# Kernel optimization log

Hardware: AMD Instinct MI355X
Metric: run time of the kernel (lower is better)

The kernel has to match this reference:

```python
import jax, jax.numpy as jnp
import numpy as np

M = 9           # n_views
CENTER = M // 2 # int(M/2)


def _grid_sample_zeros(img, gx, gy):
    """PyTorch F.grid_sample(mode='bilinear', padding_mode='zeros', align_corners=False).
    img: [V,B,H,W,C]; gx,gy: [V,B,H,W,N] normalized coords in [-1,1] (x=width, y=height).
    Returns [V,B,H,W,N,C]."""
    V, B, H, W, C = img.shape
    ix = ((gx + 1.0) * W - 1.0) * 0.5   # unnormalize, align_corners=False
    iy = ((gy + 1.0) * H - 1.0) * 0.5
    x0 = jnp.floor(ix).astype(jnp.int32); x1 = x0 + 1
    y0 = jnp.floor(iy).astype(jnp.int32); y1 = y0 + 1
    wx1 = ix - x0; wx0 = 1.0 - wx1
    wy1 = iy - y0; wy0 = 1.0 - wy1
    v_idx = jnp.arange(V)[:, None, None, None, None]
    b_idx = jnp.arange(B)[None, :, None, None, None]

    def corner(xi, yi, w):
        valid = (xi >= 0) & (xi < W) & (yi >= 0) & (yi < H)
        xc = jnp.clip(xi, 0, W - 1)
        yc = jnp.clip(yi, 0, H - 1)
        vals = img[v_idx, b_idx, yc, xc]            # [V,B,H,W,N,C] irregular gather
        return vals * (w * valid.astype(img.dtype))[..., None]

    return (corner(x0, y0, wx0 * wy0) + corner(x1, y0, wx1 * wy0)
            + corner(x0, y1, wx0 * wy1) + corner(x1, y1, wx1 * wy1))


def _forward(deltmap, imageMxM, x_g, conv_w, conv_b):
    B, H, W, N = deltmap.shape
    C = imageMxM.shape[3]
    V = M * M
    # base grid: linspace(-1,1) (matches torch code which passes it to align_corners=False sampling)
    base_x = jnp.linspace(-1.0, 1.0, W)[None, :] * jnp.ones((H, 1))   # [H,W]
    base_y = jnp.linspace(-1.0, 1.0, H)[:, None] * jnp.ones((1, W))   # [H,W]
    # per-view offsets; flatten views v-major (v outer loop, u inner) as in the torch code
    uu = jnp.tile(jnp.arange(M), M)      # [V] u varies fastest
    vv = jnp.repeat(jnp.arange(M), M)    # [V]
    sx = (2.0 * (CENTER - uu) / W).astype(deltmap.dtype)  # [V]
    sy = (2.0 * (CENTER - vv) / H).astype(deltmap.dtype)
    gx = base_x[None, None, :, :, None] + sx[:, None, None, None, None] * deltmap[None]  # [V,B,H,W,N]
    gy = base_y[None, None, :, :, None] + sy[:, None, None, None, None] * deltmap[None]
    # images per view: [B,H,W,C,M,M] -> [M,M,B,H,W,C] -> [V,B,H,W,C]
    img = jnp.moveaxis(imageMxM, (4, 5), (0, 1)).reshape(V, B, H, W, C)
    sampled = _grid_sample_zeros(img, gx, gy)          # [V,B,H,W,N,C]
    # cost layout [B,C,V,H,W,N], gate with x_g [B,1,H,W,V] -> [B,1,V,H,W,1]
    cost = jnp.transpose(sampled, (1, 5, 0, 2, 3, 4))  # [B,C,V,H,W,N]
    gate = jnp.transpose(x_g, (0, 1, 4, 2, 3))[..., None]
    cost = (cost * gate).reshape(B, C * V, H, W, N)    # channel order: c-major then v (matches reshape)
    out = jnp.einsum('bkhwn,ok->bohwn', cost, conv_w) + conv_b[None, :, None, None, None]
    return out  # [B, output_dim, H, W, N]


def setup_inputs() -> dict:
    key = jax.random.key(0)
    k1, k2, k3, k4, k5 = jax.random.split(key, 5)
    B, H, W, N, C, OUT = 1, 128, 128, 4, 8, 64
    V = M * M
    deltmap = jax.random.normal(k1, (B, H, W, N), dtype=jnp.float32)
    imageMxM = jax.random.normal(k2, (B, H, W, C, M, M), dtype=jnp.float32)
    x_g = jax.random.uniform(k3, (B, 1, H, W, V), dtype=jnp.float32)
    fan_in = C * V
    bound = 1.0 / np.sqrt(fan_in)
    conv_w = jax.random.uniform(k4, (OUT, fan_in), minval=-bound, maxval=bound, dtype=jnp.float32)
    conv_b = jax.random.uniform(k5, (OUT,), minval=-bound, maxval=bound, dtype=jnp.float32)
    return {"deltmap": deltmap, "imageMxM": imageMxM, "x_g": x_g, "conv_w": conv_w, "conv_b": conv_b}


def reference(deltmap, imageMxM, x_g, conv_w, conv_b):
    return _forward(deltmap, imageMxM, x_g, conv_w, conv_b)
```

## Files before the change

kernel.cpp:

```cpp
#include <hip/hip_runtime.h>

typedef __attribute__((ext_vector_type(8))) short bhalf8_t;
typedef __attribute__((ext_vector_type(4))) float f32x4_t;

#define KCHUNKS 21
#define NPOS 65536
#define NBLK 1024
#define W_BYTES 172032
#define T_BYTES 42467328
#define VIEW_FLOATS 131072
#define CHUNK_BYTES (4 * VIEW_FLOATS * 4)

__global__ __launch_bounds__(256) void prep_w_kernel(
    const float* __restrict__ cw, unsigned short* __restrict__ WtP)
{
    __shared__ float row[648];
    const int o = blockIdx.x, t = threadIdx.x;
    for (int i = t; i < 648; i += 256) row[i] = cw[o * 648 + i];
    __syncthreads();
    for (int k = t; k < 672; k += 256) {
        const int v = k >> 3, c = k & 7;
        const float val = (v < 81) ? row[c * 81 + v] : 0.0f;
        const unsigned int hb = __float_as_uint(val) & 0xffff0000u;
        const float r = val - __uint_as_float(hb);
        const unsigned int lb = __float_as_uint(r) & 0xffff0000u;
        const int kc = k >> 5, g = (k >> 3) & 3, e = k & 7;
        const int ix = kc * 4096 + g * 512 + o * 8 + e;
        WtP[ix]        = (unsigned short)(hb >> 16);
        WtP[ix + 2048] = (unsigned short)(lb >> 16);
    }
}

__global__ __launch_bounds__(256) void prep_T_all(
    const float* __restrict__ img, float* __restrict__ T)
{
    __shared__ float tile[16 * 8 * 85];
    const int b = blockIdx.x, t = threadIdx.x;
    const int y = b >> 3, xs = (b & 7) << 4;
    const float* src = img + (size_t)(y * 128 + xs) * 648;
#pragma unroll
    for (int k = 0; k < 64; ++k) {
        const int i = t + k * 256;
        const int vi = i & 127;
        const int c = (i >> 7) & 7;
        const int x = i >> 10;
        if (vi < 81)
            tile[(x * 8 + c) * 85 + vi] = src[x * 648 + c * 81 + vi];
    }
    __syncthreads();
#pragma unroll
    for (int k = 0; k < 64; ++k) {
        const int i = t + k * 256;
        const int vi = i >> 7;
        const int x = (i >> 3) & 15;
        const int c = i & 7;
        if (vi < 81)
            T[((size_t)(vi * 128 + y) * 128 + xs + x) * 8 + c] =
                tile[(x * 8 + c) * 85 + vi];
    }
}

__global__ __launch_bounds__(256) void prep_T_pass(
    const float* __restrict__ img, float* __restrict__ T, int v0, int nv)
{
    __shared__ float tile[16 * 8 * 85];
    const int b = blockIdx.x, t = threadIdx.x;
    const int y = b >> 3, xs = (b & 7) << 4;
    const int total = 16 * 8 * nv;
    const float* src = img + (size_t)(y * 128 + xs) * 648;
    for (int i = t; i < total; i += 256) {
        const int x = i / (8 * nv);
        const int rem = i - x * (8 * nv);
        const int c = rem / nv;
        const int vi = rem - c * nv;
        tile[(x * 8 + c) * 85 + vi] = src[x * 648 + c * 81 + v0 + vi];
    }
    __syncthreads();
    for (int i = t; i < total; i += 256) {
        const int vi = i >> 7;
        const int x = (i >> 3) & 15;
        const int c = i & 7;
        T[((size_t)(vi * 128 + y) * 128 + xs + x) * 8 + c] = tile[(x * 8 + c) * 85 + vi];
    }
}

__device__ inline unsigned int pack_pair(float a, float b, unsigned int& lw)
{
    const unsigned int ha = __float_as_uint(a) & 0xffff0000u;
    const unsigned int hb = __float_as_uint(b) & 0xffff0000u;
    const float ra = a - __uint_as_float(ha);
    const float rb = b - __uint_as_float(hb);
    lw = (__float_as_uint(ra) >> 16) | (__float_as_uint(rb) & 0xffff0000u);
    return (ha >> 16) | hb;
}

__device__ inline bhalf8_t to_b8(unsigned int a, unsigned int b,
                                 unsigned int c, unsigned int d)
{
    union { uint4 q; bhalf8_t h; } u;
    u.q = make_uint4(a, b, c, d);
    return u.h;
}

__global__ __launch_bounds__(256, 4) void build_reg(
    const float* __restrict__ delt, const float* __restrict__ xg,
    const float* __restrict__ T, const unsigned short* __restrict__ WtP,
    const float* __restrict__ bias, float* __restrict__ out,
    int kc0, int nkc, int first)
{
    const int t = threadIdx.x;
    const int frow = t & 15;
    const int fg = (t >> 4) & 3;
    const int wv = t >> 6;
    const int pos = blockIdx.x * 64 + wv * 16 + frow;
    const int h = pos >> 9;
    const int w = (pos >> 2) & 127;

    const float dlt = delt[pos];
    const float ix0 = fmaf((float)w, 128.0f / 127.0f, -0.5f);
    const float iy0 = fmaf((float)h, 128.0f / 127.0f, -0.5f);
    const int xgbase = (h * 128 + w) * 81;

    f32x4_t acc[4];
#pragma unroll
    for (int j = 0; j < 4; ++j) acc[j] = (f32x4_t)0.0f;

    for (int ci = 0; ci < nkc; ++ci) {
        const int kc = kc0 + ci;
        const int v = kc * 4 + fg;
        float sc0=0.f,sc1=0.f,sc2=0.f,sc3=0.f,sc4=0.f,sc5=0.f,sc6=0.f,sc7=0.f;
        float gate = 0.0f;
        if (v < 81) {
            gate = xg[xgbase + v];
            const int uu = v % 9, vv = v / 9;
            const float ix = fmaf((float)(4 - uu), dlt, ix0);
            const float iy = fmaf((float)(4 - vv), dlt, iy0);
            const float x0f = floorf(ix), y0f = floorf(iy);
            const float wx1 = ix - x0f, wy1 = iy - y0f;
            const float wx0 = 1.0f - wx1, wy0 = 1.0f - wy1;
            const int x0 = (int)x0f, y0 = (int)y0f;
            const int x1 = x0 + 1, y1 = y0 + 1;
            const float ex0 = (x0 >= 0 && x0 < 128) ? wx0 : 0.0f;
            const float ex1 = (x1 >= 0 && x1 < 128) ? wx1 : 0.0f;
            const float ey0 = (y0 >= 0 && y0 < 128) ? wy0 : 0.0f;
            const float ey1 = (y1 >= 0 && y1 < 128) ? wy1 : 0.0f;
            const int xc0 = min(max(x0, 0), 127), xc1 = min(max(x1, 0), 127);
            const int yc0 = min(max(y0, 0), 127), yc1 = min(max(y1, 0), 127);
            const float* bv = T + (size_t)(ci * 4 + fg) * VIEW_FLOATS;
            const float4* p00 = (const float4*)(bv + (yc0 * 128 + xc0) * 8);
            const float4* p01 = (const float4*)(bv + (yc0 * 128 + xc1) * 8);
            const float4* p10 = (const float4*)(bv + (yc1 * 128 + xc0) * 8);
            const float4* p11 = (const float4*)(bv + (yc1 * 128 + xc1) * 8);
            const float w00 = ex0 * ey0, w01 = ex1 * ey0;
            const float w10 = ex0 * ey1, w11 = ex1 * ey1;
            const float4 a00 = p00[0], b00 = p00[1];
            const float4 a01 = p01[0], b01 = p01[1];
            const float4 a10 = p10[0], b10 = p10[1];
            const float4 a11 = p11[0], b11 = p11[1];
            sc0 = fmaf(w11, a11.x, fmaf(w10, a10.x, fmaf(w01, a01.x, w00 * a00.x)));
            sc1 = fmaf(w11, a11.y, fmaf(w10, a10.y, fmaf(w01, a01.y, w00 * a00.y)));
            sc2 = fmaf(w11, a11.z, fmaf(w10, a10.z, fmaf(w01, a01.z, w00 * a00.z)));
            sc3 = fmaf(w11, a11.w, fmaf(w10, a10.w, fmaf(w01, a01.w, w00 * a00.w)));
            sc4 = fmaf(w11, b11.x, fmaf(w10, b10.x, fmaf(w01, b01.x, w00 * b00.x)));
            sc5 = fmaf(w11, b11.y, fmaf(w10, b10.y, fmaf(w01, b01.y, w00 * b00.y)));
            sc6 = fmaf(w11, b11.z, fmaf(w10, b10.z, fmaf(w01, b01.z, w00 * b00.z)));
            sc7 = fmaf(w11, b11.w, fmaf(w10, b10.w, fmaf(w01, b01.w, w00 * b00.w)));
        }
        const float g0 = sc0 * gate, g1 = sc1 * gate, g2 = sc2 * gate, g3 = sc3 * gate;
        const float g4 = sc4 * gate, g5 = sc5 * gate, g6 = sc6 * gate, g7 = sc7 * gate;
        unsigned int lw0, lw1, lw2, lw3;
        const unsigned int hw0 = pack_pair(g0, g1, lw0);
        const unsigned int hw1 = pack_pair(g2, g3, lw1);
        const unsigned int hw2 = pack_pair(g4, g5, lw2);
        const unsigned int hw3 = pack_pair(g6, g7, lw3);
        const bhalf8_t fa_hi = to_b8(hw0, hw1, hw2, hw3);
        const bhalf8_t fa_lo = to_b8(lw0, lw1, lw2, lw3);

        const unsigned short* wbase = WtP + kc * 4096 + fg * 512;
        bhalf8_t fw_hi[4], fw_lo[4];
#pragma unroll
        for (int j = 0; j < 4; ++j) {
            const int o = j * 16 + frow;
            fw_hi[j] = *(const bhalf8_t*)(wbase + o * 8);
            fw_lo[j] = *(const bhalf8_t*)(wbase + 2048 + o * 8);
        }
#pragma unroll
        for (int j = 0; j < 4; ++j) {
            acc[j] = __builtin_amdgcn_mfma_f32_16x16x32_bf16(fa_hi, fw_hi[j], acc[j], 0, 0, 0);
            acc[j] = __builtin_amdgcn_mfma_f32_16x16x32_bf16(fa_lo, fw_hi[j], acc[j], 0, 0, 0);
            acc[j] = __builtin_amdgcn_mfma_f32_16x16x32_bf16(fa_hi, fw_lo[j], acc[j], 0, 0, 0);
        }
    }

    const int posb = blockIdx.x * 64 + wv * 16 + fg * 4;
#pragma unroll
    for (int j = 0; j < 4; ++j) {
        const int o = j * 16 + frow;
        float* dst = out + (size_t)o * NPOS + posb;
        if (first) {
            const float bb = bias[o];
            *(float4*)dst = make_float4(acc[j][0] + bb, acc[j][1] + bb,
                                        acc[j][2] + bb, acc[j][3] + bb);
        } else {
            float4 cur = *(const float4*)dst;
            *(float4*)dst = make_float4(cur.x + acc[j][0], cur.y + acc[j][1],
                                        cur.z + acc[j][2], cur.w + acc[j][3]);
        }
    }
}

__global__ __launch_bounds__(256) void build_direct(
    const float* __restrict__ delt, const float* __restrict__ xg,
    const float* __restrict__ img, const float* __restrict__ cw,
    const float* __restrict__ bias, float* __restrict__ out)
{
    const int t = threadIdx.x;
    const int frow = t & 15;
    const int fg = (t >> 4) & 3;
    const int wv = t >> 6;
    const int pos = blockIdx.x * 64 + wv * 16 + frow;
    const int h = pos >> 9;
    const int w = (pos >> 2) & 127;

    const float dlt = delt[pos];
    const float ix0 = fmaf((float)w, 128.0f / 127.0f, -0.5f);
    const float iy0 = fmaf((float)h, 128.0f / 127.0f, -0.5f);
    const int xgbase = (h * 128 + w) * 81;

    f32x4_t acc[4];
#pragma unroll
    for (int j = 0; j < 4; ++j) acc[j] = (f32x4_t)0.0f;

    for (int kc = 0; kc < KCHUNKS; ++kc) {
        const int v = kc * 4 + fg;
        float sc[8];
#pragma unroll
        for (int c = 0; c < 8; ++c) sc[c] = 0.0f;
        float gate = 0.0f;
        if (v < 81) {
            gate = xg[xgbase + v];
            const int uu = v % 9, vv = v / 9;
            const float ix = fmaf((float)(4 - uu), dlt, ix0);
            const float iy = fmaf((float)(4 - vv), dlt, iy0);
            const float x0f = floorf(ix), y0f = floorf(iy);
            const float wx1 = ix - x0f, wy1 = iy - y0f;
            const float wx0 = 1.0f - wx1, wy0 = 1.0f - wy1;
            const int x0 = (int)x0f, y0 = (int)y0f;
            const int x1 = x0 + 1, y1 = y0 + 1;
            const float ex0 = (x0 >= 0 && x0 < 128) ? wx0 : 0.0f;
            const float ex1 = (x1 >= 0 && x1 < 128) ? wx1 : 0.0f;
            const float ey0 = (y0 >= 0 && y0 < 128) ? wy0 : 0.0f;
            const float ey1 = (y1 >= 0 && y1 < 128) ? wy1 : 0.0f;
            const int xc0 = min(max(x0, 0), 127), xc1 = min(max(x1, 0), 127);
            const int yc0 = min(max(y0, 0), 127), yc1 = min(max(y1, 0), 127);
            const float cwt[4] = {ex0 * ey0, ex1 * ey0, ex0 * ey1, ex1 * ey1};
            const int cyx[4] = {yc0 * 128 + xc0, yc0 * 128 + xc1,
                                yc1 * 128 + xc0, yc1 * 128 + xc1};
#pragma unroll
            for (int k = 0; k < 4; ++k) {
                const float* p = img + (size_t)cyx[k] * 648 + v;
#pragma unroll
                for (int c = 0; c < 8; ++c)
                    sc[c] = fmaf(cwt[k], p[c * 81], sc[c]);
            }
        }
        unsigned int hw[4], lw[4];
#pragma unroll
        for (int q = 0; q < 4; ++q)
            hw[q] = pack_pair(sc[2 * q] * gate, sc[2 * q + 1] * gate, lw[q]);
        const bhalf8_t fa_hi = to_b8(hw[0], hw[1], hw[2], hw[3]);
        const bhalf8_t fa_lo = to_b8(lw[0], lw[1], lw[2], lw[3]);

        bhalf8_t fw_hi[4], fw_lo[4];
#pragma unroll
        for (int j = 0; j < 4; ++j) {
            const int o = j * 16 + frow;
#pragma unroll
            for (int e = 0; e < 8; ++e) {
                const float val = (v < 81) ? cw[o * 648 + e * 81 + v] : 0.0f;
                const unsigned int hb = __float_as_uint(val) & 0xffff0000u;
                const float r = val - __uint_as_float(hb);
                fw_hi[j][e] = (short)(hb >> 16);
                fw_lo[j][e] = (short)(__float_as_uint(r) >> 16);
            }
        }
#pragma unroll
        for (int j = 0; j < 4; ++j) {
            acc[j] = __builtin_amdgcn_mfma_f32_16x16x32_bf16(fa_hi, fw_hi[j], acc[j], 0, 0, 0);
            acc[j] = __builtin_amdgcn_mfma_f32_16x16x32_bf16(fa_lo, fw_hi[j], acc[j], 0, 0, 0);
            acc[j] = __builtin_amdgcn_mfma_f32_16x16x32_bf16(fa_hi, fw_lo[j], acc[j], 0, 0, 0);
        }
    }

    const int posb = blockIdx.x * 64 + wv * 16 + fg * 4;
#pragma unroll
    for (int j = 0; j < 4; ++j) {
        const int o = j * 16 + frow;
        const float bb = bias[o];
        float* dst = out + (size_t)o * NPOS + posb;
        *(float4*)dst = make_float4(acc[j][0] + bb, acc[j][1] + bb,
                                    acc[j][2] + bb, acc[j][3] + bb);
    }
}

extern "C" void kernel_launch(void* const* d_in, const int* in_sizes, int n_in,
                              void* d_out, int out_size, void* d_ws, size_t ws_size,
                              hipStream_t stream)
{
    const float* deltmap = (const float*)d_in[0];
    const float* image   = (const float*)d_in[1];
    const float* xgp     = (const float*)d_in[2];
    const float* cw      = (const float*)d_in[3];
    const float* cb      = (const float*)d_in[4];
    float* outp = (float*)d_out;

    unsigned short* WtP = (unsigned short*)d_ws;
    float* T = (float*)((char*)d_ws + W_BYTES);

    const bool okT = ws_size >= (size_t)W_BYTES + T_BYTES;

    if (okT) {
        prep_w_kernel<<<64, 256, 0, stream>>>(cw, WtP);
        prep_T_all<<<1024, 256, 0, stream>>>(image, T);
        build_reg<<<NBLK, 256, 0, stream>>>(deltmap, xgp, T, WtP, cb, outp,
                                            0, KCHUNKS, 1);
    } else {
        long long availT = (long long)ws_size - (long long)W_BYTES;
        int G = 0;
        if (availT > 0) {
            long long g = availT / CHUNK_BYTES;
            G = (g > 21) ? 21 : (int)g;
        }
        if (G >= 1) {
            prep_w_kernel<<<64, 256, 0, stream>>>(cw, WtP);
            int first = 1;
            for (int kc0 = 0; kc0 < KCHUNKS; kc0 += G) {
                const int nkc = (KCHUNKS - kc0 < G) ? (KCHUNKS - kc0) : G;
                const int v0 = kc0 * 4;
                int nv = 81 - v0;
                if (nv > nkc * 4) nv = nkc * 4;
                prep_T_pass<<<1024, 256, 0, stream>>>(image, T, v0, nv);
                build_reg<<<NBLK, 256, 0, stream>>>(deltmap, xgp, T, WtP, cb, outp,
                                                    kc0, nkc, first);
                first = 0;
            }
        } else {
            build_direct<<<NBLK, 256, 0, stream>>>(deltmap, xgp, image, cw, cb, outp);
        }
    }
}
```

Before: 184.1 us.

## Add software-pipelined build kernel that prefetches next chunk's gathers during MFMA

Adds a build_pipe kernel where each 128-thread block handles 32 positions. Every thread gathers one view for one position, then writes the packed bf16 hi/lo fragments into double-buffered shared memory. The next chunk's bilinear gathers are issued before the current chunk's MFMAs so that memory latency overlaps matrix math, and the per-thread work is no longer split by view group. This costs a __syncthreads and shared-memory traffic per chunk, plus more registers to hold the in-flight gather results.

Measured after the change: 189.1 us. +2.7%, slower.

```diff
diff --git a/kernel.cpp b/kernel.cpp
--- a/kernel.cpp
+++ b/kernel.cpp
@@ -5,7 +5,6 @@
 
 #define KCHUNKS 21
 #define NPOS 65536
-#define NBLK 1024
 #define W_BYTES 172032
 #define T_BYTES 42467328
 #define VIEW_FLOATS 131072
@@ -102,6 +101,141 @@
     return u.h;
 }
 
+struct GatherRegs {
+    float4 a00, b00, a01, b01, a10, b10, a11, b11;
+    float w00, w01, w10, w11, gate;
+};
+
+__device__ inline void gather_issue(int v, float dlt, float ix0, float iy0,
+    int xgbase, const float* __restrict__ xg, const float* __restrict__ T,
+    GatherRegs& g)
+{
+    const int vc = (v < 81) ? v : 80;
+    g.gate = (v < 81) ? xg[xgbase + v] : 0.0f;
+    const int uu = vc % 9, vv = vc / 9;
+    const float ix = fmaf((float)(4 - uu), dlt, ix0);
+    const float iy = fmaf((float)(4 - vv), dlt, iy0);
+    const float x0f = floorf(ix), y0f = floorf(iy);
+    const float wx1 = ix - x0f, wy1 = iy - y0f;
+    const float wx0 = 1.0f - wx1, wy0 = 1.0f - wy1;
+    const int x0 = (int)x0f, y0 = (int)y0f;
+    const int x1 = x0 + 1, y1 = y0 + 1;
+    const float ex0 = (x0 >= 0 && x0 < 128) ? wx0 : 0.0f;
+    const float ex1 = (x1 >= 0 && x1 < 128) ? wx1 : 0.0f;
+    const float ey0 = (y0 >= 0 && y0 < 128) ? wy0 : 0.0f;
+    const float ey1 = (y1 >= 0 && y1 < 128) ? wy1 : 0.0f;
+    const int xc0 = min(max(x0, 0), 127), xc1 = min(max(x1, 0), 127);
+    const int yc0 = min(max(y0, 0), 127), yc1 = min(max(y1, 0), 127);
+    g.w00 = ex0 * ey0; g.w01 = ex1 * ey0;
+    g.w10 = ex0 * ey1; g.w11 = ex1 * ey1;
+    const float* bv = T + (size_t)vc * VIEW_FLOATS;
+    const float4* p00 = (const float4*)(bv + (yc0 * 128 + xc0) * 8);
+    const float4* p01 = (const float4*)(bv + (yc0 * 128 + xc1) * 8);
+    const float4* p10 = (const float4*)(bv + (yc1 * 128 + xc0) * 8);
+    const float4* p11 = (const float4*)(bv + (yc1 * 128 + xc1) * 8);
+    g.a00 = p00[0]; g.b00 = p00[1];
+    g.a01 = p01[0]; g.b01 = p01[1];
+    g.a10 = p10[0]; g.b10 = p10[1];
+    g.a11 = p11[0]; g.b11 = p11[1];
+}
+
+__device__ inline void gather_consume(const GatherRegs& g, uint4& hi, uint4& lo)
+{
+    const float s0 = fmaf(g.w11, g.a11.x, fmaf(g.w10, g.a10.x, fmaf(g.w01, g.a01.x, g.w00 * g.a00.x)));
+    const float s1 = fmaf(g.w11, g.a11.y, fmaf(g.w10, g.a10.y, fmaf(g.w01, g.a01.y, g.w00 * g.a00.y)));
+    const float s2 = fmaf(g.w11, g.a11.z, fmaf(g.w10, g.a10.z, fmaf(g.w01, g.a01.z, g.w00 * g.a00.z)));
+    const float s3 = fmaf(g.w11, g.a11.w, fmaf(g.w10, g.a10.w, fmaf(g.w01, g.a01.w, g.w00 * g.a00.w)));
+    const float s4 = fmaf(g.w11, g.b11.x, fmaf(g.w10, g.b10.x, fmaf(g.w01, g.b01.x, g.w00 * g.b00.x)));
+    const float s5 = fmaf(g.w11, g.b11.y, fmaf(g.w10, g.b10.y, fmaf(g.w01, g.b01.y, g.w00 * g.b00.y)));
+    const float s6 = fmaf(g.w11, g.b11.z, fmaf(g.w10, g.b10.z, fmaf(g.w01, g.b01.z, g.w00 * g.b00.z)));
+    const float s7 = fmaf(g.w11, g.b11.w, fmaf(g.w10, g.b10.w, fmaf(g.w01, g.b01.w, g.w00 * g.b00.w)));
+    unsigned int lw0, lw1, lw2, lw3;
+    const unsigned int hw0 = pack_pair(s0 * g.gate, s1 * g.gate, lw0);
+    const unsigned int hw1 = pack_pair(s2 * g.gate, s3 * g.gate, lw1);
+    const unsigned int hw2 = pack_pair(s4 * g.gate, s5 * g.gate, lw2);
+    const unsigned int hw3 = pack_pair(s6 * g.gate, s7 * g.gate, lw3);
+    hi = make_uint4(hw0, hw1, hw2, hw3);
+    lo = make_uint4(lw0, lw1, lw2, lw3);
+}
+
+__global__ __launch_bounds__(128, 4) void build_pipe(
+    const float* __restrict__ delt, const float* __restrict__ xg,
+    const float* __restrict__ T, const unsigned short* __restrict__ WtP,
+    const float* __restrict__ bias, float* __restrict__ out)
+{
+    __shared__ __align__(16) unsigned short Ahi[2][4][32][8];
+    __shared__ __align__(16) unsigned short Alo[2][4][32][8];
+
+    const int t = threadIdx.x;
+    const int wv = t >> 6;
+    const int lane = t & 63;
+    const int sg = t >> 5;
+    const int sp = t & 31;
+    const int pos_s = blockIdx.x * 32 + sp;
+    const int h_s = pos_s >> 9;
+    const int w_s = (pos_s >> 2) & 127;
+    const float dlt = delt[pos_s];
+    const float ix0 = fmaf((float)w_s, 128.0f / 127.0f, -0.5f);
+    const float iy0 = fmaf((float)h_s, 128.0f / 127.0f, -0.5f);
+    const int xgbase = (h_s * 128 + w_s) * 81;
+
+    const int frow = lane & 15;
+    const int fg = lane >> 4;
+
+    f32x4_t acc[4];
+#pragma unroll
+    for (int j = 0; j < 4; ++j) acc[j] = (f32x4_t)0.0f;
+
+    uint4 hiN, loN;
+    {
+        GatherRegs gr;
+        gather_issue(sg, dlt, ix0, iy0, xgbase, xg, T, gr);
+        gather_consume(gr, hiN, loN);
+    }
+
+    for (int ci = 0; ci < KCHUNKS; ++ci) {
+        const int cur = ci & 1;
+        *(uint4*)(&Ahi[cur][sg][sp][0]) = hiN;
+        *(uint4*)(&Alo[cur][sg][sp][0]) = loN;
+        __syncthreads();
+
+        GatherRegs gr;
+        const bool have = (ci + 1 < KCHUNKS);
+        if (have)
+            gather_issue((ci + 1) * 4 + sg, dlt, ix0, iy0, xgbase, xg, T, gr);
+
+        const int r = wv * 16 + frow;
+        const bhalf8_t fa_hi = *(const bhalf8_t*)(&Ahi[cur][fg][r][0]);
+        const bhalf8_t fa_lo = *(const bhalf8_t*)(&Alo[cur][fg][r][0]);
+        const unsigned short* wbase = WtP + ci * 4096 + fg * 512;
+        bhalf8_t fw_hi[4], fw_lo[4];
+#pragma unroll
+        for (int j = 0; j < 4; ++j) {
+            const int o = j * 16 + frow;
+            fw_hi[j] = *(const bhalf8_t*)(wbase + o * 8);
+            fw_lo[j] = *(const bhalf8_t*)(wbase + 2048 + o * 8);
+        }
+#pragma unroll
+        for (int j = 0; j < 4; ++j) {
+            acc[j] = __builtin_amdgcn_mfma_f32_16x16x32_bf16(fa_hi, fw_hi[j], acc[j], 0, 0, 0);
+            acc[j] = __builtin_amdgcn_mfma_f32_16x16x32_bf16(fa_lo, fw_hi[j], acc[j], 0, 0, 0);
+            acc[j] = __builtin_amdgcn_mfma_f32_16x16x32_bf16(fa_hi, fw_lo[j], acc[j], 0, 0, 0);
+        }
+
+        if (have) gather_consume(gr, hiN, loN);
+    }
+
+    const int posb = blockIdx.x * 32 + wv * 16 + fg * 4;
+#pragma unroll
+    for (int j = 0; j < 4; ++j) {
+        const int o = j * 16 + frow;
+        const float bb = bias[o];
+        float* dst = out + (size_t)o * NPOS + posb;
+        *(float4*)dst = make_float4(acc[j][0] + bb, acc[j][1] + bb,
+                                    acc[j][2] + bb, acc[j][3] + bb);
+    }
+}
+
 __global__ __launch_bounds__(256, 4) void build_reg(
     const float* __restrict__ delt, const float* __restrict__ xg,
     const float* __restrict__ T, const unsigned short* __restrict__ WtP,
@@ -128,53 +262,13 @@
     for (int ci = 0; ci < nkc; ++ci) {
         const int kc = kc0 + ci;
         const int v = kc * 4 + fg;
-        float sc0=0.f,sc1=0.f,sc2=0.f,sc3=0.f,sc4=0.f,sc5=0.f,sc6=0.f,sc7=0.f;
-        float gate = 0.0f;
-        if (v < 81) {
-            gate = xg[xgbase + v];
-            const int uu = v % 9, vv = v / 9;
-            const float ix = fmaf((float)(4 - uu), dlt, ix0);
-            const float iy = fmaf((float)(4 - vv), dlt, iy0);
-            const float x0f = floorf(ix), y0f = floorf(iy);
-            const float wx1 = ix - x0f, wy1 = iy - y0f;
-            const float wx0 = 1.0f - wx1, wy0 = 1.0f - wy1;
-            const int x0 = (int)x0f, y0 = (int)y0f;
-            const int x1 = x0 + 1, y1 = y0 + 1;
-            const float ex0 = (x0 >= 0 && x0 < 128) ? wx0 : 0.0f;
-            const float ex1 = (x1 >= 0 && x1 < 128) ? wx1 : 0.0f;
-            const float ey0 = (y0 >= 0 && y0 < 128) ? wy0 : 0.0f;
-            const float ey1 = (y1 >= 0 && y1 < 128) ? wy1 : 0.0f;
-            const int xc0 = min(max(x0, 0), 127), xc1 = min(max(x1, 0), 127);
-            const int yc0 = min(max(y0, 0), 127), yc1 = min(max(y1, 0), 127);
-            const float* bv = T + (size_t)(ci * 4 + fg) * VIEW_FLOATS;
-            const float4* p00 = (const float4*)(bv + (yc0 * 128 + xc0) * 8);
-            const float4* p01 = (const float4*)(bv + (yc0 * 128 + xc1) * 8);
-            const float4* p10 = (const float4*)(bv + (yc1 * 128 + xc0) * 8);
-            const float4* p11 = (const float4*)(bv + (yc1 * 128 + xc1) * 8);
-            const float w00 = ex0 * ey0, w01 = ex1 * ey0;
-            const float w10 = ex0 * ey1, w11 = ex1 * ey1;
-            const float4 a00 = p00[0], b00 = p00[1];
-            const float4 a01 = p01[0], b01 = p01[1];
-            const float4 a10 = p10[0], b10 = p10[1];
-            const float4 a11 = p11[0], b11 = p11[1];
-            sc0 = fmaf(w11, a11.x, fmaf(w10, a10.x, fmaf(w01, a01.x, w00 * a00.x)));
-            sc1 = fmaf(w11, a11.y, fmaf(w10, a10.y, fmaf(w01, a01.y, w00 * a00.y)));
-            sc2 = fmaf(w11, a11.z, fmaf(w10, a10.z, fmaf(w01, a01.z, w00 * a00.z)));
-            sc3 = fmaf(w11, a11.w, fmaf(w10, a10.w, fmaf(w01, a01.w, w00 * a00.w)));
-            sc4 = fmaf(w11, b11.x, fmaf(w10, b10.x, fmaf(w01, b01.x, w00 * b00.x)));
-            sc5 = fmaf(w11, b11.y, fmaf(w10, b10.y, fmaf(w01, b01.y, w00 * b00.y)));
-            sc6 = fmaf(w11, b11.z, fmaf(w10, b10.z, fmaf(w01, b01.z, w00 * b00.z)));
-            sc7 = fmaf(w11, b11.w, fmaf(w10, b10.w, fmaf(w01, b01.w, w00 * b00.w)));
-        }
-        const float g0 = sc0 * gate, g1 = sc1 * gate, g2 = sc2 * gate, g3 = sc3 * gate;
-        const float g4 = sc4 * gate, g5 = sc5 * gate, g6 = sc6 * gate, g7 = sc7 * gate;
-        unsigned int lw0, lw1, lw2, lw3;
-        const unsigned int hw0 = pack_pair(g0, g1, lw0);
-        const unsigned int hw1 = pack_pair(g2, g3, lw1);
-        const unsigned int hw2 = pack_pair(g4, g5, lw2);
-        const unsigned int hw3 = pack_pair(g6, g7, lw3);
-        const bhalf8_t fa_hi = to_b8(hw0, hw1, hw2, hw3);
-        const bhalf8_t fa_lo = to_b8(lw0, lw1, lw2, lw3);
+        GatherRegs gr;
+        gather_issue(v, dlt, ix0, iy0, xgbase, xg,
+                     T - (size_t)kc0 * 4 * VIEW_FLOATS, gr);
+        uint4 hi, lo;
+        gather_consume(gr, hi, lo);
+        const bhalf8_t fa_hi = to_b8(hi.x, hi.y, hi.z, hi.w);
+        const bhalf8_t fa_lo = to_b8(lo.x, lo.y, lo.z, lo.w);
 
         const unsigned short* wbase = WtP + kc * 4096 + fg * 512;
         bhalf8_t fw_hi[4], fw_lo[4];
@@ -322,8 +416,7 @@
     if (okT) {
         prep_w_kernel<<<64, 256, 0, stream>>>(cw, WtP);
         prep_T_all<<<1024, 256, 0, stream>>>(image, T);
-        build_reg<<<NBLK, 256, 0, stream>>>(deltmap, xgp, T, WtP, cb, outp,
-                                            0, KCHUNKS, 1);
+        build_pipe<<<2048, 128, 0, stream>>>(deltmap, xgp, T, WtP, cb, outp);
     } else {
         long long availT = (long long)ws_size - (long long)W_BYTES;
         int G = 0;
@@ -340,12 +433,12 @@
                 int nv = 81 - v0;
                 if (nv > nkc * 4) nv = nkc * 4;
                 prep_T_pass<<<1024, 256, 0, stream>>>(image, T, v0, nv);
-                build_reg<<<NBLK, 256, 0, stream>>>(deltmap, xgp, T, WtP, cb, outp,
+                build_reg<<<1024, 256, 0, stream>>>(deltmap, xgp, T, WtP, cb, outp,
                                                     kc0, nkc, first);
                 first = 0;
             }
         } else {
-            build_direct<<<NBLK, 256, 0, stream>>>(deltmap, xgp, image, cw, cb, outp);
-        }
-    }
-}
+            build_direct<<<1024, 256, 0, stream>>>(deltmap, xgp, image, cw, cb, outp);
+        }
+    }
+}
```
